# Optimization experiments

Measured on AMD Instinct MI355X. Metric: run time of the kernel, lower is better.

## Reference

```python
import jax, jax.numpy as jnp
import numpy as np

B, N, D, H, DH, DFF = 2, 2048, 1024, 16, 64, 4096
EPS = 1e-5  # F.layer_norm default


def setup_inputs() -> dict:
    key = jax.random.key(0)
    ks = jax.random.split(key, 8)
    w = lambda k, shape: jax.random.normal(k, shape, dtype=jnp.float32) * 0.02
    # standard rotary frequencies over full head dim (rot_dim = DH)
    inv_freq = 1.0 / (10000.0 ** (jnp.arange(0, DH, 2, dtype=jnp.float32) / DH))
    t = jnp.arange(N, dtype=jnp.float32)
    f = t[:, None] * inv_freq[None, :]          # [N, DH/2]
    freqs = jnp.concatenate([f, f], axis=-1)    # [N, DH]
    return {
        "x": jax.random.normal(ks[0], (B, N, D), dtype=jnp.float32),
        "gamma_pre": jnp.ones((D,), jnp.float32),
        "w_qkv": w(ks[1], (3 * D, D)),
        "w_o": w(ks[2], (D, D)),
        "gamma_ff": jnp.ones((D,), jnp.float32),
        "w_up": w(ks[3], (DFF, D)),
        "b_up": jnp.zeros((DFF,), jnp.float32),
        "w_gate": w(ks[4], (DFF, D)),
        "b_gate": jnp.zeros((DFF,), jnp.float32),
        "w_out": w(ks[5], (D, DFF)),
        "b_out": jnp.zeros((D,), jnp.float32),
        "freqs": freqs,
        "mask": jnp.ones((B, N), dtype=bool),
    }


def _layernorm(x, gamma):
    mu = jnp.mean(x, axis=-1, keepdims=True)
    var = jnp.var(x, axis=-1, keepdims=True)
    return (x - mu) * jax.lax.rsqrt(var + EPS) * gamma


def _rotate_half(x):
    x1, x2 = jnp.split(x, 2, axis=-1)
    return jnp.concatenate([-x2, x1], axis=-1)


def _rope(t, freqs):
    # rot_dim == DH so nothing is left unrotated
    return t * jnp.cos(freqs) + _rotate_half(t) * jnp.sin(freqs)


def reference(x, gamma_pre, w_qkv, w_o, gamma_ff, w_up, b_up, w_gate, b_gate,
              w_out, b_out, freqs, mask):
    b, n, d = x.shape
    # ---- self-attention branch (pre-norm) ----
    h = _layernorm(x, gamma_pre)
    qkv = h @ w_qkv.T                                   # [b, n, 3d]
    q, k, v = jnp.split(qkv, 3, axis=-1)
    to_heads = lambda t: t.reshape(b, n, H, DH).transpose(0, 2, 1, 3)  # b h n d
    q, k, v = to_heads(q), to_heads(k), to_heads(v)
    q = _rope(q, freqs)
    k = _rope(k, freqs)
    scale = 1.0 / np.sqrt(DH).astype(np.float32)
    dots = jnp.einsum('bhid,bhjd->bhij', q, k) * scale  # [b, H, n, n]
    neg = -jnp.finfo(dots.dtype).max
    dots = jnp.where(mask[:, None, None, :], dots, neg)        # key padding mask
    causal = jnp.triu(jnp.ones((n, n), dtype=bool), 1)
    dots = jnp.where(causal, neg, dots)
    attn = jax.nn.softmax(dots.astype(jnp.float32), axis=-1).astype(dots.dtype)
    o = jnp.einsum('bhij,bhjd->bhid', attn, v)
    o = o.transpose(0, 2, 1, 3).reshape(b, n, d) @ w_o.T
    o = jnp.where(mask[..., None], o, 0.0)
    x = x + o
    # ---- GLU feed-forward branch (pre-norm) ----
    h2 = _layernorm(x, gamma_ff)
    up = h2 @ w_up.T + b_up
    gate = h2 @ w_gate.T + b_gate
    ff = (up * jax.nn.silu(gate)) @ w_out.T + b_out
    return x + ff
```

## Files before the change

kernel.cpp:

```cpp
#include <hip/hip_runtime.h>
#include <stdint.h>


#define B_ 2
#define N_ 2048
#define D_ 1024
#define H_ 16
#define DFF_ 4096
#define ROWS_ (B_*N_)

typedef unsigned short u16;
typedef short short4_ __attribute__((ext_vector_type(4)));
typedef short short8 __attribute__((ext_vector_type(8)));
typedef float float4_ __attribute__((ext_vector_type(4)));

#define NEGBIG (-1e30f)
#define QSCALE 0.1803368801111204f

__device__ __forceinline__ float b2f(u16 u) {
  union { unsigned u; float f; } c; c.u = ((unsigned)u) << 16; return c.f;
}
__device__ __forceinline__ u16 f2b(float f) {
  union { float f; unsigned u; } c; c.f = f;
  unsigned x = c.u;
// ... 50 lines not shown
  if ((t & 63) == 0) { red[t >> 6] = s; red[4 + (t >> 6)] = ss; }
  __syncthreads();
  s  = red[0] + red[1] + red[2] + red[3];
  ss = red[4] + red[5] + red[6] + red[7];
  float mu  = s * (1.f / D_);
  float var = ss * (1.f / D_) - mu * mu;
  float rs  = rsqrtf(var + 1e-5f);
#pragma unroll
  for (int i = 0; i < 4; i++)
    out[(size_t)row * D_ + t * 4 + i] = f2b((v[i] - mu) * rs * gamma[t * 4 + i]);
}

__global__ __launch_bounds__(256) void combine_ln(const u16* p0,
                                                  const u16* __restrict__ p1,
                                                  const float* __restrict__ resid,
                                                  const float* __restrict__ gamma,
                                                  float* __restrict__ x1,
                                                  u16* h2out) {
  int row = blockIdx.x, t = threadIdx.x;
  size_t base = (size_t)row * D_ + t * 4;
  short4_ a = *(const short4_*)(p0 + base);
  short4_ b = *(const short4_*)(p1 + base);
  float4_ rv = *(const float4_*)(resid + base);
  float4_ v;
  float s = 0.f, ss = 0.f;
#pragma unroll
  for (int i = 0; i < 4; i++) {
    v[i] = b2f((u16)a[i]) + b2f((u16)b[i]) + rv[i];
    s += v[i]; ss += v[i] * v[i];
  }
  *(float4_*)(x1 + base) = v;
#pragma unroll
  for (int off = 1; off < 64; off <<= 1) {
    s  += __shfl_xor(s, off, 64);
    ss += __shfl_xor(ss, off, 64);
  }
  __shared__ float red[8];
  if ((t & 63) == 0) { red[t >> 6] = s; red[4 + (t >> 6)] = ss; }
  __syncthreads();
  s  = red[0] + red[1] + red[2] + red[3];
  ss = red[4] + red[5] + red[6] + red[7];
  float mu  = s * (1.f / D_);
  float var = ss * (1.f / D_) - mu * mu;
  float rs  = rsqrtf(var + 1e-5f);
#pragma unroll
  for (int i = 0; i < 4; i++)
    h2out[base + i] = f2b((v[i] - mu) * rs * gamma[t * 4 + i]);
}

template <int MODE>
__device__ __forceinline__ void gemm_epilogue(float4_ (&acc)[4][4], void* Cout,
                                              const float* bias, const void* extra,
                                              int mbase, int nbase, int N,
                                              int wr, int wc, int quad, int l16) {
#pragma unroll
  for (int i = 0; i < 4; i++) {
#pragma unroll
    for (int r = 0; r < 4; r++) {
      int row = mbase + wr * 64 + i * 16 + quad * 4 + r;
#pragma unroll
      for (int j = 0; j < 4; j++) {
        int col = nbase + wc * 64 + j * 16 + l16;
        size_t idx = (size_t)row * N + col;
        float v = acc[i][j][r];
        if (MODE == 0) {
          ((u16*)Cout)[idx] = f2b(v);
        } else if (MODE == 1) {
          ((u16*)Cout)[idx] = f2b(v + bias[col]);
        } else if (MODE == 2) {
          ((float*)Cout)[idx] = v + ((const float*)extra)[idx];
        } else if (MODE == 3) {
          float gate = v + bias[col];
          float sig = 1.f / (1.f + expf(-gate));
          float upv = b2f(((const u16*)extra)[idx]);
          ((u16*)Cout)[idx] = f2b(upv * gate * sig);
        } else {
          ((float*)Cout)[idx] = v + bias[col] + ((const float*)extra)[idx];
        }
      }
    }
  }
}

__device__ __forceinline__ void gemm_core64(const u16* A, const u16* W,
                                            float4_ (&acc)[4][4], u16* sA, u16* sW,
                                            int mbase, int nbase, int K,
                                            int klo, int khi,
                                            int wave, int lane, int wr, int wc,
                                            int quad, int l16) {
  int colb = ((lane & 3) ^ ((lane >> 3) & 3)) << 3;
  int qs8  = (quad ^ ((l16 >> 1) & 3)) * 8;
  for (int k0 = klo; k0 < khi; k0 += 64) {
    __syncthreads();
#pragma unroll
    for (int hh = 0; hh < 2; hh++) {
      int kh = k0 + hh * 32;
#pragma unroll
      for (int it = 0; it < 2; it++) {
        int c = wave * 128 + it * 64 + lane;
        int row = c >> 2;
        gl_lds16(A + (size_t)(mbase + row) * K + kh + colb,
                 sA + hh * 4096 + (size_t)(wave * 128 + it * 64) * 8);
        gl_lds16(W + (size_t)(nbase + row) * K + kh + colb,
                 sW + hh * 4096 + (size_t)(wave * 128 + it * 64) * 8);
      }
    }
    __syncthreads();
#pragma unroll
    for (int hh = 0; hh < 2; hh++) {
      const u16* sAp = sA + hh * 4096;
      const u16* sWp = sW + hh * 4096;
      short8 af[4], bf[4];
#pragma unroll
      for (int i = 0; i < 4; i++)
        af[i] = *(const short8*)(sAp + (wr * 64 + i * 16 + l16) * 32 + qs8);
#pragma unroll
      for (int j = 0; j < 4; j++)
        bf[j] = *(const short8*)(sWp + (wc * 64 + j * 16 + l16) * 32 + qs8);
#pragma unroll
      for (int i = 0; i < 4; i++)
#pragma unroll
        for (int j = 0; j < 4; j++)
          acc[i][j] = __builtin_amdgcn_mfma_f32_16x16x32_bf16(af[i], bf[j], acc[i][j], 0, 0, 0);
    }
  }
}

__device__ __forceinline__ void glu8_stageA(const u16* A, u16* aslot, int mbase,
                                            int kk, int wave, int lane, int colb) {
  int rw = wave * 16 + (lane >> 2);
#pragma unroll
  for (int it = 0; it < 2; it++) {
    int row = it * 128 + rw;
    gl_lds16(A + (size_t)(mbase + row) * 1024 + kk * 32 + colb,
             aslot + it * 4096 + wave * 512);
  }
}
__device__ __forceinline__ void glu8_stageB(const u16* Wu, const u16* Wg, u16* bslot,
                                            int nbase, int kk, int wave, int lane,
                                            int colb) {
  int rw = wave * 16 + (lane >> 2);
  size_t go = (size_t)(nbase + rw) * 1024 + kk * 32 + colb;
  gl_lds16(Wu + go, bslot + wave * 512);
  gl_lds16(Wg + go, bslot + 4096 + wave * 512);
}

__global__ __launch_bounds__(512) void gemm_glu8(const u16* __restrict__ A,
                                                 const u16* __restrict__ Wu,
                                                 const u16* __restrict__ Wg,
                                                 const float* __restrict__ bu,
                                                 const float* __restrict__ bg,
                                                 u16* __restrict__ G) {
  __shared__ __align__(16) u16 ring[4][16384];
  const int NT = 32;
  int t_ = threadIdx.x, wave = t_ >> 6, lane = t_ & 63;
  int wr = wave >> 2, wc = wave & 3;
  int quad = lane >> 4, l16 = lane & 15;
  int mbase = blockIdx.y * 256, nbase = blockIdx.x * 128;
  int colb = ((lane & 3) ^ ((lane >> 3) & 3)) << 3;
  int qs8  = (quad ^ ((l16 >> 1) & 3)) * 8;

  float4_ z4 = {0.f, 0.f, 0.f, 0.f};
  float4_ acc[8][4];
#pragma unroll
  for (int i = 0; i < 8; i++)
#pragma unroll
    for (int j = 0; j < 4; j++) acc[i][j] = z4;

#pragma unroll
  for (int kk = 0; kk < 3; kk++) {
    glu8_stageA(A, ring[kk], mbase, kk, wave, lane, colb);
    glu8_stageB(Wu, Wg, ring[kk] + 8192, nbase, kk, wave, lane, colb);
  }

  for (int t = 0; t < NT; t++) {
    if (t < NT - 2)       asm volatile("s_waitcnt vmcnt(8)" ::: "memory");
    else if (t == NT - 2) asm volatile("s_waitcnt vmcnt(4)" ::: "memory");
    else                  asm volatile("s_waitcnt vmcnt(0)" ::: "memory");
    __builtin_amdgcn_s_barrier();
    asm volatile("" ::: "memory");

    const u16* as = ring[t & 3];
    const u16* bs = as + 8192;
    bool prefetch = (t + 3 < NT);
    int kk = t + 3;

    if (prefetch) glu8_stageA(A, ring[kk & 3], mbase, kk, wave, lane, colb);
    short8 af[4], bf[4];
#pragma unroll
    for (int i = 0; i < 4; i++)
      af[i] = *(const short8*)(as + (wr * 128 + i * 16 + l16) * 32 + qs8);
#pragma unroll
    for (int j = 0; j < 4; j++)
      bf[j] = *(const short8*)(bs + (wc * 64 + j * 16 + l16) * 32 + qs8);
    __builtin_amdgcn_s_setprio(1);
#pragma unroll
    for (int i = 0; i < 4; i++)
#pragma unroll
      for (int j = 0; j < 4; j++)
        acc[i][j] = __builtin_amdgcn_mfma_f32_16x16x32_bf16(af[i], bf[j], acc[i][j], 0, 0, 0);
    __builtin_amdgcn_s_setprio(0);
    __builtin_amdgcn_s_barrier();
    asm volatile("" ::: "memory");

    if (prefetch) glu8_stageB(Wu, Wg, ring[kk & 3] + 8192, nbase, kk, wave, lane, colb);
    short8 ag[4];
#pragma unroll
    for (int i = 0; i < 4; i++)
      ag[i] = *(const short8*)(as + (wr * 128 + (4 + i) * 16 + l16) * 32 + qs8);
    __builtin_amdgcn_s_setprio(1);
#pragma unroll
    for (int i = 0; i < 4; i++)
#pragma unroll
      for (int j = 0; j < 4; j++)
        acc[4 + i][j] = __builtin_amdgcn_mfma_f32_16x16x32_bf16(ag[i], bf[j], acc[4 + i][j], 0, 0, 0);
    __builtin_amdgcn_s_setprio(0);
  }

  __syncthreads();
  u16* ex = &ring[0][0];
  if (wc >= 2) {
    int cc = (wc - 2) * 64;
#pragma unroll
    for (int i = 0; i < 8; i++)
#pragma unroll
      for (int r = 0; r < 4; r++) {
        int row = wr * 128 + i * 16 + quad * 4 + r;
#pragma unroll
        for (int j = 0; j < 4; j++) {
          int col = cc + j * 16 + l16;
          float gv = acc[i][j][r] + bg[nbase + col];
          float sig = 1.f / (1.f + expf(-gv));
          ex[row * 128 + col] = f2b(gv * sig);
        }
      }
  }
  __syncthreads();
  if (wc < 2) {
    int cc = wc * 64;
#pragma unroll
    for (int i = 0; i < 8; i++)
#pragma unroll
      for (int r = 0; r < 4; r++) {
        int row = wr * 128 + i * 16 + quad * 4 + r;
#pragma unroll
        for (int j = 0; j < 4; j++) {
          int col = cc + j * 16 + l16;
          float uv = acc[i][j][r] + bu[nbase + col];
          G[(size_t)(mbase + row) * DFF_ + nbase + col] =
              f2b(uv * b2f(ex[row * 128 + col]));
        }
      }
  }
}

__global__ __launch_bounds__(256) void gemm_bb_split(const u16* __restrict__ A,
                                                     const u16* __restrict__ W,
                                                     u16* __restrict__ p0,
                                                     u16* __restrict__ p1,
                                                     int M, int N, int K) {
  __shared__ __align__(16) u16 sA[2][128 * 32];
  __shared__ __align__(16) u16 sW[2][128 * 32];
  int t = threadIdx.x;
  int mbase = blockIdx.y * 128, nbase = blockIdx.x * 128;
  int z = blockIdx.z;
  int wave = t >> 6, lane = t & 63;
  int wr = wave >> 1, wc = wave & 1;
  int quad = lane >> 4, l16 = lane & 15;
  int Kh = K >> 1;

  float4_ z4 = {0.f, 0.f, 0.f, 0.f};
  float4_ acc[4][4];
#pragma unroll
  for (int i = 0; i < 4; i++)
#pragma unroll
    for (int j = 0; j < 4; j++) acc[i][j] = z4;

  gemm_core64(A, W, acc, &sA[0][0], &sW[0][0], mbase, nbase, K,
              z * Kh, z * Kh + Kh, wave, lane, wr, wc, quad, l16);

  u16* P = z ? p1 : p0;
#pragma unroll
  for (int i = 0; i < 4; i++)
#pragma unroll
    for (int r = 0; r < 4; r++) {
      int row = mbase + wr * 64 + i * 16 + quad * 4 + r;
#pragma unroll
      for (int j = 0; j < 4; j++) {
        int col = nbase + wc * 64 + j * 16 + l16;
        P[(size_t)row * N + col] = f2b(acc[i][j][r]);
      }
    }
}

__global__ __launch_bounds__(256) void split_combine(const u16* __restrict__ p0,
                                                     const u16* __restrict__ p1,
                                                     const float* __restrict__ bias,
                                                     const float* __restrict__ resid,
                                                     float* __restrict__ out, int N) {
  int idx = (blockIdx.x * 256 + threadIdx.x) * 8;
  int col = idx & (N - 1);
  short8 a = *(const short8*)(p0 + idx);
  short8 b = *(const short8*)(p1 + idx);
  float4_ r0 = *(const float4_*)(resid + idx);
  float4_ r1 = *(const float4_*)(resid + idx + 4);
  float4_ o0, o1;
#pragma unroll
  for (int e = 0; e < 4; e++) {
    float bb0 = bias ? bias[col + e] : 0.f;
    float bb1 = bias ? bias[col + 4 + e] : 0.f;
    o0[e] = b2f((u16)a[e]) + b2f((u16)b[e]) + bb0 + r0[e];
    o1[e] = b2f((u16)a[4 + e]) + b2f((u16)b[4 + e]) + bb1 + r1[e];
  }
  *(float4_*)(out + idx) = o0;
  *(float4_*)(out + idx + 4) = o1;
}

template <int MODE>
__global__ __launch_bounds__(256) void gemm_nt(const u16* __restrict__ A,
                                               const float* __restrict__ W,
                                               void* Cout,
                                               const float* __restrict__ bias,
                                               const void* extra,
                                               int M, int N, int K) {
  __shared__ __align__(16) u16 sA[128 * 32];
  __shared__ __align__(16) u16 sW[128 * 32];
  int t = threadIdx.x;
  int mbase = blockIdx.y * 128, nbase = blockIdx.x * 128;
  int wave = t >> 6, lane = t & 63;
  int wr = wave >> 1, wc = wave & 1;
  int quad = lane >> 4, l16 = lane & 15;

  float4_ z4 = {0.f, 0.f, 0.f, 0.f};
  float4_ acc[4][4];
#pragma unroll
  for (int i = 0; i < 4; i++)
#pragma unroll
    for (int j = 0; j < 4; j++) acc[i][j] = z4;

  for (int k0 = 0; k0 < K; k0 += 32) {
    __syncthreads();
#pragma unroll
    for (int it = 0; it < 2; it++) {
      int c = t + 256 * it;
      int row = c >> 2, col = (c & 3) << 3;
      ((short8*)sA)[c] = *(const short8*)(A + (size_t)(mbase + row) * K + k0 + col);
      const float* wp = W + (size_t)(nbase + row) * K + k0 + col;
      float4_ w0 = *(const float4_*)wp;
      float4_ w1 = *(const float4_*)(wp + 4);
      short8 pk;
#pragma unroll
      for (int e = 0; e < 4; e++) { pk[e] = (short)f2b(w0[e]); pk[4 + e] = (short)f2b(w1[e]); }
      ((short8*)sW)[c] = pk;
    }
    __syncthreads();
    short8 af[4], bf[4];
#pragma unroll
    for (int i = 0; i < 4; i++)
      af[i] = *(const short8*)(sA + (wr * 64 + i * 16 + l16) * 32 + quad * 8);
#pragma unroll
    for (int j = 0; j < 4; j++)
      bf[j] = *(const short8*)(sW + (wc * 64 + j * 16 + l16) * 32 + quad * 8);
#pragma unroll
    for (int i = 0; i < 4; i++)
#pragma unroll
      for (int j = 0; j < 4; j++)
        acc[i][j] = __builtin_amdgcn_mfma_f32_16x16x32_bf16(af[i], bf[j], acc[i][j], 0, 0, 0);
  }
  gemm_epilogue<MODE>(acc, Cout, bias, extra, mbase, nbase, N, wr, wc, quad, l16);
}

template <int SPLIT>
__global__ __launch_bounds__(256) void rope_kernel(const u16* __restrict__ q0,
                                                   const u16* __restrict__ q1,
                                                   const float* __restrict__ freqs,
                                                   u16* __restrict__ qr,
                                                   u16* __restrict__ kr,
                                                   u16* __restrict__ vt) {
  int idx = blockIdx.x * 256 + threadIdx.x;
  int d2 = idx & 31;
  int h  = (idx >> 5) & 15;
  int n  = (idx >> 9) & 2047;
  int b  = idx >> 20;
  float f = freqs[n * 64 + d2];
  float c = cosf(f), s = sinf(f);
  size_t base = (size_t)(b * N_ + n) * 3072;
  int hd = h * 64 + d2;
#define LD(o) (SPLIT ? (b2f(q0[base + (o)]) + b2f(q1[base + (o)])) : b2f(q0[base + (o)]))
  float v_q1 = LD(hd),        v_q2 = LD(hd + 32);
  float v_k1 = LD(1024 + hd), v_k2 = LD(1024 + hd + 32);
  float v_v1 = LD(2048 + hd), v_v2 = LD(2048 + hd + 32);
#undef LD
  size_t ro = ((size_t)(b * H_ + h) * N_ + n) * 64 + d2;
  qr[ro]      = f2b((v_q1 * c - v_q2 * s) * QSCALE);
  qr[ro + 32] = f2b((v_q2 * c + v_q1 * s) * QSCALE);
  kr[ro]      = f2b(v_k1 * c - v_k2 * s);
  kr[ro + 32] = f2b(v_k2 * c + v_k1 * s);
  size_t vo = ((size_t)(b * H_ + h) * 64 + d2) * N_ + n;
  vt[vo]           = f2b(v_v1);
  vt[vo + 32 * N_] = f2b(v_v2);
}

#define LP 72
#define NSPLIT 4
__global__ __launch_bounds__(256) void attn_kernel(const u16* __restrict__ qr,
                                                   const u16* __restrict__ kr,
                                                   const u16* __restrict__ vt,
                                                   u16* __restrict__ opart,
                                                   float* __restrict__ mlp) {
  __shared__ __align__(16) u16 sK[64 * LP];
  __shared__ __align__(16) u16 sV[64 * LP];
  __shared__ __align__(16) u16 sP[4][16 * LP];
  int qp = blockIdx.x, bh = blockIdx.y, sp = blockIdx.z;
  int t = threadIdx.x, wave = t >> 6, lane = t & 63;
  int quad = lane >> 4, l16 = lane & 15;
  const u16* qptr = qr + (size_t)bh * N_ * 64;
  const u16* kp = kr + (size_t)bh * N_ * 64;
  const u16* vp = vt + (size_t)bh * 64 * N_;
  float4_ z4 = {0.f, 0.f, 0.f, 0.f};

  for (int qsel = 0; qsel < 2; qsel++) {
    int qt = qsel ? (N_ / 64 - 1 - qp) : qp;
    int qbase = qt * 64;
    int ntiles = qt + 1;
    int ktlo = (ntiles * sp) / NSPLIT, kthi = (ntiles * (sp + 1)) / NSPLIT;

    short8 aq[2];
    int qrow = qbase + wave * 16 + l16;
#pragma unroll
    for (int kk = 0; kk < 2; kk++)
      aq[kk] = *(const short8*)(qptr + (size_t)qrow * 64 + kk * 32 + quad * 8);

    float4_ o[4] = {z4, z4, z4, z4};
    float m_r[4] = {NEGBIG, NEGBIG, NEGBIG, NEGBIG};
    float l_r[4] = {0.f, 0.f, 0.f, 0.f};

    for (int kt = ktlo; kt < kthi; kt++) {
      __syncthreads();
      {
        const u16* src = kp + (size_t)kt * 64 * 64;
#pragma unroll
        for (int it = 0; it < 2; it++) {
          int c = t + 256 * it;
          int row = c >> 3, seg = c & 7;
          *(short8*)(sK + row * LP + seg * 8) = *(const short8*)(src + c * 8);
          *(short8*)(sV + row * LP + seg * 8) =
              *(const short8*)(vp + (size_t)row * N_ + kt * 64 + seg * 8);
        }
      }
      __syncthreads();

      float4_ sf[4];
#pragma unroll
      for (int j = 0; j < 4; j++) {
        short8 bk0 = *(const short8*)(sK + (j * 16 + l16) * LP + quad * 8);
        short8 bk1 = *(const short8*)(sK + (j * 16 + l16) * LP + 32 + quad * 8);
        float4_ acc = z4;
        acc = __builtin_amdgcn_mfma_f32_16x16x32_bf16(aq[0], bk0, acc, 0, 0, 0);
        acc = __builtin_amdgcn_mfma_f32_16x16x32_bf16(aq[1], bk1, acc, 0, 0, 0);
        sf[j] = acc;
      }
      if (kt == qt) {
#pragma unroll
        for (int j = 0; j < 4; j++)
#pragma unroll
          for (int r = 0; r < 4; r++) {
            int ig = qbase + wave * 16 + quad * 4 + r;
            int jg = kt * 64 + j * 16 + l16;
            if (jg > ig) sf[j][r] = NEGBIG;
          }
      }

#pragma unroll
      for (int r = 0; r < 4; r++) {
        float mt = fmaxf(fmaxf(sf[0][r], sf[1][r]), fmaxf(sf[2][r], sf[3][r]));
#pragma unroll
        for (int off = 1; off < 16; off <<= 1) mt = fmaxf(mt, __shfl_xor(mt, off, 64));
        float mn = fmaxf(m_r[r], mt);
        float alpha = exp2f(m_r[r] - mn);
        float rowsum = 0.f;
#pragma unroll
        for (int j = 0; j < 4; j++) {
          float p = exp2f(sf[j][r] - mn);
          sf[j][r] = p;
          rowsum += p;
        }
#pragma unroll
        for (int off = 1; off < 16; off <<= 1) rowsum += __shfl_xor(rowsum, off, 64);
        l_r[r] = l_r[r] * alpha + rowsum;
        m_r[r] = mn;
#pragma unroll
        for (int jo = 0; jo < 4; jo++) o[jo][r] *= alpha;
      }

      u16* sPw = sP[wave];
#pragma unroll
      for (int j = 0; j < 4; j++)
#pragma unroll
        for (int r = 0; r < 4; r++)
          sPw[(quad * 4 + r) * LP + j * 16 + l16] = f2b(sf[j][r]);
      short8 ap[2];
#pragma unroll
      for (int kk = 0; kk < 2; kk++)
        ap[kk] = *(const short8*)(sPw + l16 * LP + kk * 32 + quad * 8);
#pragma unroll
      for (int jo = 0; jo < 4; jo++)
#pragma unroll
        for (int kk = 0; kk < 2; kk++) {
          short8 bv = *(const short8*)(sV + (jo * 16 + l16) * LP + kk * 32 + quad * 8);
          o[jo] = __builtin_amdgcn_mfma_f32_16x16x32_bf16(ap[kk], bv, o[jo], 0, 0, 0);
        }
    }

#pragma unroll
    for (int r = 0; r < 4; r++) {
      int n = qbase + wave * 16 + quad * 4 + r;
      size_t row = (size_t)bh * N_ + n;
      if (l16 == 0) {
        mlp[2 * (sp * (size_t)65536 + row)]     = m_r[r];
        mlp[2 * (sp * (size_t)65536 + row) + 1] = l_r[r];
      }
#pragma unroll
      for (int jo = 0; jo < 4; jo++)
        opart[sp * (size_t)4194304 + row * 64 + jo * 16 + l16] = f2b(o[jo][r]);
    }
  }
}

__global__ __launch_bounds__(256) void attn_combine(const u16* __restrict__ opart,
                                                    const float* __restrict__ mlp,
                                                    u16* __restrict__ obuf) {
  int idx = blockIdx.x * 256 + threadIdx.x;
  int row = idx >> 3, seg = idx & 7;
  float mm[NSPLIT], ll[NSPLIT];
  float mmax = NEGBIG;
#pragma unroll
  for (int s = 0; s < NSPLIT; s++) {
    mm[s] = mlp[2 * (s * (size_t)65536 + row)];
    ll[s] = mlp[2 * (s * (size_t)65536 + row) + 1];
    mmax = fmaxf(mmax, mm[s]);
  }
  float w[NSPLIT], lsum = 0.f;
#pragma unroll
  for (int s = 0; s < NSPLIT; s++) { w[s] = exp2f(mm[s] - mmax); lsum += ll[s] * w[s]; }
  float inv = 1.f / lsum;
  float acc[8] = {0, 0, 0, 0, 0, 0, 0, 0};
#pragma unroll
  for (int s = 0; s < NSPLIT; s++) {
    short8 a = *(const short8*)(opart + s * (size_t)4194304 + (size_t)row * 64 + seg * 8);
#pragma unroll
    for (int e = 0; e < 8; e++) acc[e] += b2f((u16)a[e]) * w[s];
  }
  short8 r;
#pragma unroll
  for (int e = 0; e < 8; e++) r[e] = (short)f2b(acc[e] * inv);
  int bh = row >> 11, n = row & 2047;
  int bb = bh >> 4, h = bh & 15;
  *(short8*)(obuf + ((size_t)(bb * N_ + n) * D_) + h * 64 + seg * 8) = r;
}

extern "C" void kernel_launch(void* const* d_in, const int* in_sizes, int n_in,
                              void* d_out, int out_size, void* d_ws, size_t ws_size,
                              hipStream_t stream) {
  const float* x         = (const float*)d_in[0];
  const float* gamma_pre = (const float*)d_in[1];
  const float* w_qkv     = (const float*)d_in[2];
  const float* w_o       = (const float*)d_in[3];
  const float* gamma_ff  = (const float*)d_in[4];
  const float* w_up      = (const float*)d_in[5];
  const float* b_up      = (const float*)d_in[6];
  const float* w_gate    = (const float*)d_in[7];
  const float* b_gate    = (const float*)d_in[8];
  const float* w_out     = (const float*)d_in[9];
  const float* b_out     = (const float*)d_in[10];
  const float* freqs     = (const float*)d_in[11];

  char* ws = (char*)d_ws;
  const size_t MB = 1024 * 1024;
  float* out = (float*)d_out;
  bool wide = ws_size >= 96 * MB;

  if (wide) {
    u16*  h     = (u16*)(ws);
    u16*  qp0   = (u16*)(ws + 8 * MB);
    u16*  qp1   = (u16*)(ws + 32 * MB);
    u16*  qr    = (u16*)(ws + 56 * MB);
    u16*  kr    = (u16*)d_out;
    u16*  vtb   = (u16*)d_out + 4194304;
    u16*  opart = (u16*)(ws);
    float* mlb  = (float*)(ws + 32 * MB);
    u16*  ob    = (u16*)(ws + 34 * MB);
    u16*  sp0   = (u16*)(ws);
    u16*  sp1o  = (u16*)(ws + 8 * MB);
    float* x1   = (float*)(ws + 16 * MB);
    u16*  h2    = (u16*)(ws);
    u16*  g     = (u16*)(ws + 32 * MB);
    u16*  sp0f  = (u16*)(ws);
    u16*  sp1f  = (u16*)(ws + 8 * MB);
    u16* wb_qkv  = (u16*)(ws + 64 * MB);
    u16* wb_o    = (u16*)(ws + 70 * MB);
    u16* wb_up   = (u16*)(ws + 72 * MB);
    u16* wb_gate = (u16*)(ws + 80 * MB);
    u16* wb_out  = (u16*)(ws + 88 * MB);

    cvt_all<<<8192, 256, 0, stream>>>(w_qkv, w_o, w_up, w_gate, w_out,
                                      wb_qkv, wb_o, wb_up, wb_gate, wb_out);
    ln_kernel<<<ROWS_, 256, 0, stream>>>(x, gamma_pre, h);
    gemm_bb_split<<<dim3(3072 / 128, ROWS_ / 128, 2), 256, 0, stream>>>(
        h, wb_qkv, qp0, qp1, ROWS_, 3072, 1024);
    rope_kernel<1><<<(B_ * N_ * H_ * 32) / 256, 256, 0, stream>>>(
        qp0, qp1, freqs, qr, kr, vtb);
    attn_kernel<<<dim3(N_ / 128, B_ * H_, NSPLIT), 256, 0, stream>>>(
        qr, kr, vtb, opart, mlb);
    attn_combine<<<(B_ * H_ * N_ * 8) / 256, 256, 0, stream>>>(opart, mlb, ob);
    gemm_bb_split<<<dim3(1024 / 128, ROWS_ / 128, 2), 256, 0, stream>>>(
        ob, wb_o, sp0, sp1o, ROWS_, 1024, 1024);
    combine_ln<<<ROWS_, 256, 0, stream>>>(sp0, sp1o, x, gamma_ff, x1, h2);
    gemm_glu8<<<dim3(DFF_ / 128, ROWS_ / 256), 512, 0, stream>>>(
        h2, wb_up, wb_gate, b_up, b_gate, g);
    gemm_bb_split<<<dim3(1024 / 128, ROWS_ / 128, 2), 256, 0, stream>>>(
        g, wb_out, sp0f, sp1f, ROWS_, 1024, 4096);
    split_combine<<<(ROWS_ * 1024) / 2048, 256, 0, stream>>>(
        sp0f, sp1f, b_out, x1, out, 1024);
  } else {
    u16*  h     = (u16*)(ws);
    u16*  qkv   = (u16*)(ws + 8 * MB);
    u16*  qr    = (u16*)(ws + 32 * MB);
    u16*  kr    = (u16*)(ws + 40 * MB);
    u16*  vtb   = (u16*)(ws + 48 * MB);
    u16*  ob    = (u16*)(ws + 56 * MB);
    float* x1   = (float*)(ws + 8 * MB);
    u16*  h2    = (u16*)(ws + 24 * MB);
    u16*  g     = (u16*)(ws + 32 * MB);

    ln_kernel<<<ROWS_, 256, 0, stream>>>(x, gamma_pre, h);
    gemm_nt<0><<<dim3(3072 / 128, ROWS_ / 128), 256, 0, stream>>>(
        h, w_qkv, qkv, nullptr, nullptr, ROWS_, 3072, 1024);
    rope_kernel<0><<<(B_ * N_ * H_ * 32) / 256, 256, 0, stream>>>(
        qkv, qkv, freqs, qr, kr, vtb);
    attn_kernel<<<dim3(N_ / 128, B_ * H_, NSPLIT), 256, 0, stream>>>(
        qr, kr, vtb, (u16*)(ws), (float*)(ws + 32 * MB));
    attn_combine<<<(B_ * H_ * N_ * 8) / 256, 256, 0, stream>>>(
        (u16*)(ws), (float*)(ws + 32 * MB), ob);
    gemm_nt<2><<<dim3(1024 / 128, ROWS_ / 128), 256, 0, stream>>>(
        ob, w_o, x1, nullptr, x, ROWS_, 1024, 1024);
    ln_kernel<<<ROWS_, 256, 0, stream>>>(x1, gamma_ff, h2);
    gemm_nt<1><<<dim3(4096 / 128, ROWS_ / 128), 256, 0, stream>>>(
        h2, w_up, g, b_up, nullptr, ROWS_, 4096, 1024);
    gemm_nt<3><<<dim3(4096 / 128, ROWS_ / 128), 256, 0, stream>>>(
        h2, w_gate, g, b_gate, g, ROWS_, 4096, 1024);
    gemm_nt<4><<<dim3(1024 / 128, ROWS_ / 128), 256, 0, stream>>>(
        g, w_out, (void*)out, b_out, x1, ROWS_, 1024, 4096);
  }
}
```

Measured before the change: 458.3 us.

## Pipeline split-K GEMM with 4-slot LDS ring and register double-buffered fragments

The split-K GEMM used for the QKV, O and FF-out projections is rebuilt. Instead of a two-barrier load-then-compute loop, it now uses a 4-slot LDS ring with three stages of direct global-to-LDS prefetch and counted vmcnt waits. The GLU GEMM keeps its 4-slot ring, but both kernels now read the next stage's fragments into a second register set while the MFMAs of the current stage run, so LDS reads overlap compute. This costs more registers and LDS, which may lower occupancy.

After: 471.0 us. +2.8%, slower.

```diff
diff --git a/kernel.cpp b/kernel.cpp
--- a/kernel.cpp
+++ b/kernel.cpp
@@ -156,67 +156,97 @@
   }
 }
 
-__device__ __forceinline__ void gemm_core64(const u16* A, const u16* W,
-                                            float4_ (&acc)[4][4], u16* sA, u16* sW,
-                                            int mbase, int nbase, int K,
-                                            int klo, int khi,
-                                            int wave, int lane, int wr, int wc,
-                                            int quad, int l16) {
+__global__ __launch_bounds__(256) void gemm_bb_split(const u16* __restrict__ A,
+                                                     const u16* __restrict__ W,
+                                                     u16* __restrict__ p0,
+                                                     u16* __restrict__ p1,
+                                                     int M, int N, int K) {
+  __shared__ __align__(16) u16 ring[4][8192];
+  int t_ = threadIdx.x, wave = t_ >> 6, lane = t_ & 63;
+  int wr = wave >> 1, wc = wave & 1;
+  int quad = lane >> 4, l16 = lane & 15;
+  int mbase = blockIdx.y * 128, nbase = blockIdx.x * 128;
+  int z = blockIdx.z;
+  int Kh = K >> 1, kbase = z * Kh;
+  const int NT = Kh >> 5;
   int colb = ((lane & 3) ^ ((lane >> 3) & 3)) << 3;
   int qs8  = (quad ^ ((l16 >> 1) & 3)) * 8;
-  for (int k0 = klo; k0 < khi; k0 += 64) {
-    __syncthreads();
-#pragma unroll
-    for (int hh = 0; hh < 2; hh++) {
-      int kh = k0 + hh * 32;
-#pragma unroll
-      for (int it = 0; it < 2; it++) {
-        int c = wave * 128 + it * 64 + lane;
-        int row = c >> 2;
-        gl_lds16(A + (size_t)(mbase + row) * K + kh + colb,
-                 sA + hh * 4096 + (size_t)(wave * 128 + it * 64) * 8);
-        gl_lds16(W + (size_t)(nbase + row) * K + kh + colb,
-                 sW + hh * 4096 + (size_t)(wave * 128 + it * 64) * 8);
-      }
+
+  float4_ z4 = {0.f, 0.f, 0.f, 0.f};
+  float4_ acc[4][4];
+#pragma unroll
+  for (int i = 0; i < 4; i++)
+#pragma unroll
+    for (int j = 0; j < 4; j++) acc[i][j] = z4;
+
+  auto STAGE = [&](int kk) {
+    u16* sl = &ring[kk & 3][0];
+    int kc = kbase + kk * 32 + colb;
+#pragma unroll
+    for (int it = 0; it < 2; it++) {
+      int c = it * 256 + wave * 64 + lane;
+      int row = c >> 2;
+      gl_lds16(A + (size_t)(mbase + row) * K + kc, sl + (it * 256 + wave * 64) * 8);
+      gl_lds16(W + (size_t)(nbase + row) * K + kc, sl + 4096 + (it * 256 + wave * 64) * 8);
     }
-    __syncthreads();
-#pragma unroll
-    for (int hh = 0; hh < 2; hh++) {
-      const u16* sAp = sA + hh * 4096;
-      const u16* sWp = sW + hh * 4096;
-      short8 af[4], bf[4];
-#pragma unroll
-      for (int i = 0; i < 4; i++)
-        af[i] = *(const short8*)(sAp + (wr * 64 + i * 16 + l16) * 32 + qs8);
+  };
+  auto READF = [&](short8 (&fa)[4], short8 (&fb)[4], int kk) {
+    const u16* sl = &ring[kk & 3][0];
+#pragma unroll
+    for (int i = 0; i < 4; i++)
+      fa[i] = *(const short8*)(sl + (wr * 64 + i * 16 + l16) * 32 + qs8);
+#pragma unroll
+    for (int j = 0; j < 4; j++)
+      fb[j] = *(const short8*)(sl + 4096 + (wc * 64 + j * 16 + l16) * 32 + qs8);
+  };
+  auto MM = [&](short8 (&fa)[4], short8 (&fb)[4]) {
+    __builtin_amdgcn_s_setprio(1);
+#pragma unroll
+    for (int i = 0; i < 4; i++)
 #pragma unroll
       for (int j = 0; j < 4; j++)
-        bf[j] = *(const short8*)(sWp + (wc * 64 + j * 16 + l16) * 32 + qs8);
-#pragma unroll
-      for (int i = 0; i < 4; i++)
-#pragma unroll
-        for (int j = 0; j < 4; j++)
-          acc[i][j] = __builtin_amdgcn_mfma_f32_16x16x32_bf16(af[i], bf[j], acc[i][j], 0, 0, 0);
+        acc[i][j] = __builtin_amdgcn_mfma_f32_16x16x32_bf16(fa[i], fb[j], acc[i][j], 0, 0, 0);
+    __builtin_amdgcn_s_setprio(0);
+  };
+
+  STAGE(0); STAGE(1); STAGE(2);
+  asm volatile("s_waitcnt vmcnt(8)" ::: "memory");
+  __builtin_amdgcn_s_barrier();
+  asm volatile("" ::: "memory");
+  short8 aX[4], bX[4], aY[4], bY[4];
+  READF(aX, bX, 0);
+
+  auto ITER = [&](int t, short8 (&ca)[4], short8 (&cb)[4],
+                  short8 (&na)[4], short8 (&nb)[4]) {
+    if (t + 3 < NT) STAGE(t + 3);
+    if (t + 1 < NT) {
+      if (t + 3 < NT)      asm volatile("s_waitcnt vmcnt(8)" ::: "memory");
+      else if (t + 2 < NT) asm volatile("s_waitcnt vmcnt(4)" ::: "memory");
+      else                 asm volatile("s_waitcnt vmcnt(0)" ::: "memory");
+      __builtin_amdgcn_s_barrier();
+      asm volatile("" ::: "memory");
+      READF(na, nb, t + 1);
     }
-  }
-}
-
-__device__ __forceinline__ void glu8_stageA(const u16* A, u16* aslot, int mbase,
-                                            int kk, int wave, int lane, int colb) {
-  int rw = wave * 16 + (lane >> 2);
-#pragma unroll
-  for (int it = 0; it < 2; it++) {
-    int row = it * 128 + rw;
-    gl_lds16(A + (size_t)(mbase + row) * 1024 + kk * 32 + colb,
-             aslot + it * 4096 + wave * 512);
-  }
-}
-__device__ __forceinline__ void glu8_stageB(const u16* Wu, const u16* Wg, u16* bslot,
-                                            int nbase, int kk, int wave, int lane,
-                                            int colb) {
-  int rw = wave * 16 + (lane >> 2);
-  size_t go = (size_t)(nbase + rw) * 1024 + kk * 32 + colb;
-  gl_lds16(Wu + go, bslot + wave * 512);
-  gl_lds16(Wg + go, bslot + 4096 + wave * 512);
+    MM(ca, cb);
+    if (t + 1 < NT) { __builtin_amdgcn_s_barrier(); asm volatile("" ::: "memory"); }
+  };
+  for (int t = 0; t < NT; t += 2) {
+    ITER(t, aX, bX, aY, bY);
+    ITER(t + 1, aY, bY, aX, bX);
+  }
+
+  u16* P = z ? p1 : p0;
+#pragma unroll
+  for (int i = 0; i < 4; i++)
+#pragma unroll
+    for (int r = 0; r < 4; r++) {
+      int row = mbase + wr * 64 + i * 16 + quad * 4 + r;
+#pragma unroll
+      for (int j = 0; j < 4; j++) {
+        int col = nbase + wc * 64 + j * 16 + l16;
+        P[(size_t)row * N + col] = f2b(acc[i][j][r]);
+      }
+    }
 }
 
 __global__ __launch_bounds__(512) void gemm_glu8(const u16* __restrict__ A,
@@ -241,54 +271,62 @@
 #pragma unroll
     for (int j = 0; j < 4; j++) acc[i][j] = z4;
 
-#pragma unroll
-  for (int kk = 0; kk < 3; kk++) {
-    glu8_stageA(A, ring[kk], mbase, kk, wave, lane, colb);
-    glu8_stageB(Wu, Wg, ring[kk] + 8192, nbase, kk, wave, lane, colb);
-  }
-
-  for (int t = 0; t < NT; t++) {
-    if (t < NT - 2)       asm volatile("s_waitcnt vmcnt(8)" ::: "memory");
-    else if (t == NT - 2) asm volatile("s_waitcnt vmcnt(4)" ::: "memory");
-    else                  asm volatile("s_waitcnt vmcnt(0)" ::: "memory");
-    __builtin_amdgcn_s_barrier();
-    asm volatile("" ::: "memory");
-
-    const u16* as = ring[t & 3];
+  auto STAGE = [&](int kk) {
+    u16* sl = &ring[kk & 3][0];
+    int rw = wave * 16 + (lane >> 2);
+    int kc = kk * 32 + colb;
+#pragma unroll
+    for (int it = 0; it < 2; it++)
+      gl_lds16(A + (size_t)(mbase + it * 128 + rw) * 1024 + kc,
+               sl + it * 4096 + wave * 512);
+    size_t go = (size_t)(nbase + rw) * 1024 + kc;
+    gl_lds16(Wu + go, sl + 8192 + wave * 512);
+    gl_lds16(Wg + go, sl + 12288 + wave * 512);
+  };
+  auto READF = [&](short8 (&fa)[8], short8 (&fb)[4], int kk) {
+    const u16* as = &ring[kk & 3][0];
     const u16* bs = as + 8192;
-    bool prefetch = (t + 3 < NT);
-    int kk = t + 3;
-
-    if (prefetch) glu8_stageA(A, ring[kk & 3], mbase, kk, wave, lane, colb);
-    short8 af[4], bf[4];
-#pragma unroll
-    for (int i = 0; i < 4; i++)
-      af[i] = *(const short8*)(as + (wr * 128 + i * 16 + l16) * 32 + qs8);
+#pragma unroll
+    for (int i = 0; i < 8; i++)
+      fa[i] = *(const short8*)(as + (wr * 128 + i * 16 + l16) * 32 + qs8);
 #pragma unroll
     for (int j = 0; j < 4; j++)
-      bf[j] = *(const short8*)(bs + (wc * 64 + j * 16 + l16) * 32 + qs8);
+      fb[j] = *(const short8*)(bs + (wc * 64 + j * 16 + l16) * 32 + qs8);
+  };
+  auto MM = [&](short8 (&fa)[8], short8 (&fb)[4]) {
     __builtin_amdgcn_s_setprio(1);
 #pragma unroll
-    for (int i = 0; i < 4; i++)
+    for (int i = 0; i < 8; i++)
 #pragma unroll
       for (int j = 0; j < 4; j++)
-        acc[i][j] = __builtin_amdgcn_mfma_f32_16x16x32_bf16(af[i], bf[j], acc[i][j], 0, 0, 0);
+        acc[i][j] = __builtin_amdgcn_mfma_f32_16x16x32_bf16(fa[i], fb[j], acc[i][j], 0, 0, 0);
     __builtin_amdgcn_s_setprio(0);
-    __builtin_amdgcn_s_barrier();
-    asm volatile("" ::: "memory");
-
-    if (prefetch) glu8_stageB(Wu, Wg, ring[kk & 3] + 8192, nbase, kk, wave, lane, colb);
-    short8 ag[4];
-#pragma unroll
-    for (int i = 0; i < 4; i++)
-      ag[i] = *(const short8*)(as + (wr * 128 + (4 + i) * 16 + l16) * 32 + qs8);
-    __builtin_amdgcn_s_setprio(1);
-#pragma unroll
-    for (int i = 0; i < 4; i++)
-#pragma unroll
-      for (int j = 0; j < 4; j++)
-        acc[4 + i][j] = __builtin_amdgcn_mfma_f32_16x16x32_bf16(ag[i], bf[j], acc[4 + i][j], 0, 0, 0);
-    __builtin_amdgcn_s_setprio(0);
+  };
+
+  STAGE(0); STAGE(1); STAGE(2);
+  asm volatile("s_waitcnt vmcnt(8)" ::: "memory");
+  __builtin_amdgcn_s_barrier();
+  asm volatile("" ::: "memory");
+  short8 aX[8], bX[4], aY[8], bY[4];
+  READF(aX, bX, 0);
+
+  auto ITER = [&](int t, short8 (&ca)[8], short8 (&cb)[4],
+                  short8 (&na)[8], short8 (&nb)[4]) {
+    if (t + 3 < NT) STAGE(t + 3);
+    if (t + 1 < NT) {
+      if (t + 3 < NT)      asm volatile("s_waitcnt vmcnt(8)" ::: "memory");
+      else if (t + 2 < NT) asm volatile("s_waitcnt vmcnt(4)" ::: "memory");
+      else                 asm volatile("s_waitcnt vmcnt(0)" ::: "memory");
+      __builtin_amdgcn_s_barrier();
+      asm volatile("" ::: "memory");
+      READF(na, nb, t + 1);
+    }
+    MM(ca, cb);
+    if (t + 1 < NT) { __builtin_amdgcn_s_barrier(); asm volatile("" ::: "memory"); }
+  };
+  for (int t = 0; t < NT; t += 2) {
+    ITER(t, aX, bX, aY, bY);
+    ITER(t + 1, aY, bY, aX, bX);
   }
 
   __syncthreads();
@@ -326,45 +364,6 @@
         }
       }
   }
-}
-
-__global__ __launch_bounds__(256) void gemm_bb_split(const u16* __restrict__ A,
-                                                     const u16* __restrict__ W,
-                                                     u16* __restrict__ p0,
-                                                     u16* __restrict__ p1,
-                                                     int M, int N, int K) {
-  __shared__ __align__(16) u16 sA[2][128 * 32];
-  __shared__ __align__(16) u16 sW[2][128 * 32];
-  int t = threadIdx.x;
-  int mbase = blockIdx.y * 128, nbase = blockIdx.x * 128;
-  int z = blockIdx.z;
-  int wave = t >> 6, lane = t & 63;
-  int wr = wave >> 1, wc = wave & 1;
-  int quad = lane >> 4, l16 = lane & 15;
-  int Kh = K >> 1;
-
-  float4_ z4 = {0.f, 0.f, 0.f, 0.f};
-  float4_ acc[4][4];
-#pragma unroll
-  for (int i = 0; i < 4; i++)
-#pragma unroll
-    for (int j = 0; j < 4; j++) acc[i][j] = z4;
-
-  gemm_core64(A, W, acc, &sA[0][0], &sW[0][0], mbase, nbase, K,
-              z * Kh, z * Kh + Kh, wave, lane, wr, wc, quad, l16);
-
-  u16* P = z ? p1 : p0;
-#pragma unroll
-  for (int i = 0; i < 4; i++)
-#pragma unroll
-    for (int r = 0; r < 4; r++) {
-      int row = mbase + wr * 64 + i * 16 + quad * 4 + r;
-#pragma unroll
-      for (int j = 0; j < 4; j++) {
-        int col = nbase + wc * 64 + j * 16 + l16;
-        P[(size_t)row * N + col] = f2b(acc[i][j][r]);
-      }
-    }
 }
 
 __global__ __launch_bounds__(256) void split_combine(const u16* __restrict__ p0,
```

## Double-buffer K/V tiles in attention and remap GEMM block order

Applied to the files above, without the earlier changes.

The attention kernel now prefetches the next K/V tile into registers while computing on the current one, using two LDS buffers, so global load latency overlaps with MFMA work. The number of block barriers per tile stays about the same. The split GEMM and GLU GEMM kernels remap linear block IDs so that groups of 8 consecutive blocks land on different N-columns with the same M-row tiles. This is meant to improve L2 reuse, possibly per-XCD locality. The cost is more register pressure from the prefetched short8 values and extra LDS for the second buffer.

Result: slower. 468.4 us (+2.2%).

```diff
diff --git a/kernel.cpp b/kernel.cpp
--- a/kernel.cpp
+++ b/kernel.cpp
@@ -200,6 +200,50 @@
   }
 }
 
+__global__ __launch_bounds__(256) void gemm_bb_split(const u16* __restrict__ A,
+                                                     const u16* __restrict__ W,
+                                                     u16* __restrict__ p0,
+                                                     u16* __restrict__ p1,
+                                                     int M, int N, int K,
+                                                     int GXC) {
+  __shared__ __align__(16) u16 sA[2][128 * 32];
+  __shared__ __align__(16) u16 sW[2][128 * 32];
+  int t = threadIdx.x;
+  int b = blockIdx.y * (GXC * 8) + blockIdx.x;
+  int grp = b >> 3;
+  int xs = (b & 7) * GXC + (grp >> 5);
+  int ys = grp & 31;
+  int mbase = ys * 128, nbase = xs * 128;
+  int z = blockIdx.z;
+  int wave = t >> 6, lane = t & 63;
+  int wr = wave >> 1, wc = wave & 1;
+  int quad = lane >> 4, l16 = lane & 15;
+  int Kh = K >> 1;
+
+  float4_ z4 = {0.f, 0.f, 0.f, 0.f};
+  float4_ acc[4][4];
+#pragma unroll
+  for (int i = 0; i < 4; i++)
+#pragma unroll
+    for (int j = 0; j < 4; j++) acc[i][j] = z4;
+
+  gemm_core64(A, W, acc, &sA[0][0], &sW[0][0], mbase, nbase, K,
+              z * Kh, z * Kh + Kh, wave, lane, wr, wc, quad, l16);
+
+  u16* P = z ? p1 : p0;
+#pragma unroll
+  for (int i = 0; i < 4; i++)
+#pragma unroll
+    for (int r = 0; r < 4; r++) {
+      int row = mbase + wr * 64 + i * 16 + quad * 4 + r;
+#pragma unroll
+      for (int j = 0; j < 4; j++) {
+        int col = nbase + wc * 64 + j * 16 + l16;
+        P[(size_t)row * N + col] = f2b(acc[i][j][r]);
+      }
+    }
+}
+
 __device__ __forceinline__ void glu8_stageA(const u16* A, u16* aslot, int mbase,
                                             int kk, int wave, int lane, int colb) {
   int rw = wave * 16 + (lane >> 2);
@@ -230,7 +274,11 @@
   int t_ = threadIdx.x, wave = t_ >> 6, lane = t_ & 63;
   int wr = wave >> 2, wc = wave & 3;
   int quad = lane >> 4, l16 = lane & 15;
-  int mbase = blockIdx.y * 256, nbase = blockIdx.x * 128;
+  int b = blockIdx.y * 32 + blockIdx.x;
+  int grp = b >> 3;
+  int xs = (b & 7) * 4 + (grp >> 4);
+  int ys = grp & 15;
+  int mbase = ys * 256, nbase = xs * 128;
   int colb = ((lane & 3) ^ ((lane >> 3) & 3)) << 3;
   int qs8  = (quad ^ ((l16 >> 1) & 3)) * 8;
 
@@ -326,45 +374,6 @@
         }
       }
   }
-}
-
-__global__ __launch_bounds__(256) void gemm_bb_split(const u16* __restrict__ A,
-                                                     const u16* __restrict__ W,
-                                                     u16* __restrict__ p0,
-                                                     u16* __restrict__ p1,
-                                                     int M, int N, int K) {
-  __shared__ __align__(16) u16 sA[2][128 * 32];
-  __shared__ __align__(16) u16 sW[2][128 * 32];
-  int t = threadIdx.x;
-  int mbase = blockIdx.y * 128, nbase = blockIdx.x * 128;
-  int z = blockIdx.z;
-  int wave = t >> 6, lane = t & 63;
-  int wr = wave >> 1, wc = wave & 1;
-  int quad = lane >> 4, l16 = lane & 15;
-  int Kh = K >> 1;
-
-  float4_ z4 = {0.f, 0.f, 0.f, 0.f};
-  float4_ acc[4][4];
-#pragma unroll
-  for (int i = 0; i < 4; i++)
-#pragma unroll
-    for (int j = 0; j < 4; j++) acc[i][j] = z4;
-
-  gemm_core64(A, W, acc, &sA[0][0], &sW[0][0], mbase, nbase, K,
-              z * Kh, z * Kh + Kh, wave, lane, wr, wc, quad, l16);
-
-  u16* P = z ? p1 : p0;
-#pragma unroll
-  for (int i = 0; i < 4; i++)
-#pragma unroll
-    for (int r = 0; r < 4; r++) {
-      int row = mbase + wr * 64 + i * 16 + quad * 4 + r;
-#pragma unroll
-      for (int j = 0; j < 4; j++) {
-        int col = nbase + wc * 64 + j * 16 + l16;
-        P[(size_t)row * N + col] = f2b(acc[i][j][r]);
-      }
-    }
 }
 
 __global__ __launch_bounds__(256) void split_combine(const u16* __restrict__ p0,
@@ -482,8 +491,8 @@
                                                    const u16* __restrict__ vt,
                                                    u16* __restrict__ opart,
                                                    float* __restrict__ mlp) {
-  __shared__ __align__(16) u16 sK[64 * LP];
-  __shared__ __align__(16) u16 sV[64 * LP];
+  __shared__ __align__(16) u16 sK[2][64 * LP];
+  __shared__ __align__(16) u16 sV[2][64 * LP];
   __shared__ __align__(16) u16 sP[4][16 * LP];
   int qp = blockIdx.x, bh = blockIdx.y, sp = blockIdx.z;
   int t = threadIdx.x, wave = t >> 6, lane = t & 63;
@@ -492,6 +501,9 @@
   const u16* kp = kr + (size_t)bh * N_ * 64;
   const u16* vp = vt + (size_t)bh * 64 * N_;
   float4_ z4 = {0.f, 0.f, 0.f, 0.f};
+  int c0 = t, c1 = t + 256;
+  int r0 = c0 >> 3, s0 = (c0 & 7) * 8;
+  int r1 = c1 >> 3, s1 = (c1 & 7) * 8;
 
   for (int qsel = 0; qsel < 2; qsel++) {
     int qt = qsel ? (N_ / 64 - 1 - qp) : qp;
@@ -509,26 +521,27 @@
     float m_r[4] = {NEGBIG, NEGBIG, NEGBIG, NEGBIG};
     float l_r[4] = {0.f, 0.f, 0.f, 0.f};
 
-    for (int kt = ktlo; kt < kthi; kt++) {
-      __syncthreads();
-      {
-        const u16* src = kp + (size_t)kt * 64 * 64;
-#pragma unroll
-        for (int it = 0; it < 2; it++) {
-          int c = t + 256 * it;
-          int row = c >> 3, seg = c & 7;
-          *(short8*)(sK + row * LP + seg * 8) = *(const short8*)(src + c * 8);
-          *(short8*)(sV + row * LP + seg * 8) =
-              *(const short8*)(vp + (size_t)row * N_ + kt * 64 + seg * 8);
-        }
-      }
-      __syncthreads();
-
+    auto LOADR = [&](short8& ka, short8& kb, short8& va, short8& vb, int kt) {
+      const u16* src = kp + (size_t)kt * 4096;
+      ka = *(const short8*)(src + c0 * 8);
+      kb = *(const short8*)(src + c1 * 8);
+      va = *(const short8*)(vp + (size_t)r0 * N_ + kt * 64 + s0);
+      vb = *(const short8*)(vp + (size_t)r1 * N_ + kt * 64 + s1);
+    };
+    auto WRITE = [&](short8& ka, short8& kb, short8& va, short8& vb, int buf) {
+      *(short8*)(sK[buf] + r0 * LP + s0) = ka;
+      *(short8*)(sK[buf] + r1 * LP + s1) = kb;
+      *(short8*)(sV[buf] + r0 * LP + s0) = va;
+      *(short8*)(sV[buf] + r1 * LP + s1) = vb;
+    };
+    auto COMPUTE = [&](int kt, int buf) {
+      const u16* sKb = sK[buf];
+      const u16* sVb = sV[buf];
       float4_ sf[4];
 #pragma unroll
       for (int j = 0; j < 4; j++) {
-        short8 bk0 = *(const short8*)(sK + (j * 16 + l16) * LP + quad * 8);
-        short8 bk1 = *(const short8*)(sK + (j * 16 + l16) * LP + 32 + quad * 8);
+        short8 bk0 = *(const short8*)(sKb + (j * 16 + l16) * LP + quad * 8);
+        short8 bk1 = *(const short8*)(sKb + (j * 16 + l16) * LP + 32 + quad * 8);
         float4_ acc = z4;
         acc = __builtin_amdgcn_mfma_f32_16x16x32_bf16(aq[0], bk0, acc, 0, 0, 0);
         acc = __builtin_amdgcn_mfma_f32_16x16x32_bf16(aq[1], bk1, acc, 0, 0, 0);
@@ -544,7 +557,6 @@
             if (jg > ig) sf[j][r] = NEGBIG;
           }
       }
-
 #pragma unroll
       for (int r = 0; r < 4; r++) {
         float mt = fmaxf(fmaxf(sf[0][r], sf[1][r]), fmaxf(sf[2][r], sf[3][r]));
@@ -566,7 +578,6 @@
 #pragma unroll
         for (int jo = 0; jo < 4; jo++) o[jo][r] *= alpha;
       }
-
       u16* sPw = sP[wave];
 #pragma unroll
       for (int j = 0; j < 4; j++)
@@ -581,9 +592,27 @@
       for (int jo = 0; jo < 4; jo++)
 #pragma unroll
         for (int kk = 0; kk < 2; kk++) {
-          short8 bv = *(const short8*)(sV + (jo * 16 + l16) * LP + kk * 32 + quad * 8);
+          short8 bv = *(const short8*)(sVb + (jo * 16 + l16) * LP + kk * 32 + quad * 8);
           o[jo] = __builtin_amdgcn_mfma_f32_16x16x32_bf16(ap[kk], bv, o[jo], 0, 0, 0);
         }
+    };
+
+    if (ktlo < kthi) {
+      short8 kA0, kA1, vA0, vA1, kB0, kB1, vB0, vB1;
+      LOADR(kA0, kA1, vA0, vA1, ktlo);
+      __syncthreads();
+      for (int kt = ktlo; kt < kthi; kt += 2) {
+        WRITE(kA0, kA1, vA0, vA1, 0);
+        if (kt + 1 < kthi) LOADR(kB0, kB1, vB0, vB1, kt + 1);
+        __syncthreads();
+        COMPUTE(kt, 0);
+        if (kt + 1 < kthi) {
+          WRITE(kB0, kB1, vB0, vB1, 1);
+          if (kt + 2 < kthi) LOADR(kA0, kA1, vA0, vA1, kt + 2);
+          __syncthreads();
+          COMPUTE(kt + 1, 1);
+        }
+      }
     }
 
 #pragma unroll
@@ -681,19 +710,19 @@
                                       wb_qkv, wb_o, wb_up, wb_gate, wb_out);
     ln_kernel<<<ROWS_, 256, 0, stream>>>(x, gamma_pre, h);
     gemm_bb_split<<<dim3(3072 / 128, ROWS_ / 128, 2), 256, 0, stream>>>(
-        h, wb_qkv, qp0, qp1, ROWS_, 3072, 1024);
+        h, wb_qkv, qp0, qp1, ROWS_, 3072, 1024, 3);
     rope_kernel<1><<<(B_ * N_ * H_ * 32) / 256, 256, 0, stream>>>(
         qp0, qp1, freqs, qr, kr, vtb);
     attn_kernel<<<dim3(N_ / 128, B_ * H_, NSPLIT), 256, 0, stream>>>(
         qr, kr, vtb, opart, mlb);
     attn_combine<<<(B_ * H_ * N_ * 8) / 256, 256, 0, stream>>>(opart, mlb, ob);
     gemm_bb_split<<<dim3(1024 / 128, ROWS_ / 128, 2), 256, 0, stream>>>(
-        ob, wb_o, sp0, sp1o, ROWS_, 1024, 1024);
+        ob, wb_o, sp0, sp1o, ROWS_, 1024, 1024, 1);
     combine_ln<<<ROWS_, 256, 0, stream>>>(sp0, sp1o, x, gamma_ff, x1, h2);
     gemm_glu8<<<dim3(DFF_ / 128, ROWS_ / 256), 512, 0, stream>>>(
         h2, wb_up, wb_gate, b_up, b_gate, g);
     gemm_bb_split<<<dim3(1024 / 128, ROWS_ / 128, 2), 256, 0, stream>>>(
-        g, wb_out, sp0f, sp1f, ROWS_, 1024, 4096);
+        g, wb_out, sp0f, sp1f, ROWS_, 1024, 4096, 1);
     split_combine<<<(ROWS_ * 1024) / 2048, 256, 0, stream>>>(
         sp0f, sp1f, b_out, x1, out, 1024);
   } else {
```

## Fuse RoPE and Q/K/V head layout into QKV GEMM epilogue, drop split-K

Applied to the files above, without the earlier changes.

Replaces the split-K QKV GEMM plus the separate rope kernel with a single GEMM that runs the full K=1024 reduction. Its epilogue applies the rotary embedding, the Q scale and the per-head layout, writing V transposed directly. This removes two bf16 partial buffers and one kernel launch. In exchange the grid has half as many blocks, the epilogue computes sin/cos per element, and the transposed V stores are strided.

Measured after the change: 623.8 us. 1.36x slower.

```diff
diff --git a/kernel.cpp b/kernel.cpp
--- a/kernel.cpp
+++ b/kernel.cpp
@@ -200,6 +200,109 @@
   }
 }
 
+__global__ __launch_bounds__(256) void gemm_qkv_rope(const u16* __restrict__ A,
+                                                     const u16* __restrict__ W,
+                                                     const float* __restrict__ freqs,
+                                                     u16* __restrict__ qr,
+                                                     u16* __restrict__ kr,
+                                                     u16* __restrict__ vt) {
+  __shared__ __align__(16) u16 sA[2][128 * 32];
+  __shared__ __align__(16) u16 sW[2][128 * 32];
+  int t = threadIdx.x;
+  int mbase = blockIdx.y * 128, nbase = blockIdx.x * 128;
+  int wave = t >> 6, lane = t & 63;
+  int wr = wave >> 1, wc = wave & 1;
+  int quad = lane >> 4, l16 = lane & 15;
+
+  float4_ z4 = {0.f, 0.f, 0.f, 0.f};
+  float4_ acc[4][4];
+#pragma unroll
+  for (int i = 0; i < 4; i++)
+#pragma unroll
+    for (int j = 0; j < 4; j++) acc[i][j] = z4;
+
+  gemm_core64(A, W, acc, &sA[0][0], &sW[0][0], mbase, nbase, 1024,
+              0, 1024, wave, lane, wr, wc, quad, l16);
+
+  int sec = nbase >> 10;
+  int hbase = ((nbase & 1023) >> 6) + wc;
+  if (sec < 2) {
+    float qs = sec == 0 ? QSCALE : 1.0f;
+    u16* dst = sec == 0 ? qr : kr;
+#pragma unroll
+    for (int i = 0; i < 4; i++) {
+#pragma unroll
+      for (int r = 0; r < 4; r++) {
+        int row = mbase + wr * 64 + i * 16 + quad * 4 + r;
+        int n = row & 2047, bsel = row >> 11;
+        float f0 = freqs[n * 64 + l16];
+        float f1 = freqs[n * 64 + 16 + l16];
+        float c0 = cosf(f0), s0 = sinf(f0);
+        float c1 = cosf(f1), s1 = sinf(f1);
+        size_t base = ((size_t)(bsel * 16 + hbase) * 2048 + n) * 64;
+        float v1a = acc[i][0][r], v2a = acc[i][2][r];
+        float v1b = acc[i][1][r], v2b = acc[i][3][r];
+        dst[base + l16]      = f2b((v1a * c0 - v2a * s0) * qs);
+        dst[base + 16 + l16] = f2b((v1b * c1 - v2b * s1) * qs);
+        dst[base + 32 + l16] = f2b((v2a * c0 + v1a * s0) * qs);
+        dst[base + 48 + l16] = f2b((v2b * c1 + v1b * s1) * qs);
+      }
+    }
+  } else {
+#pragma unroll
+    for (int i = 0; i < 4; i++) {
+#pragma unroll
+      for (int r = 0; r < 4; r++) {
+        int row = mbase + wr * 64 + i * 16 + quad * 4 + r;
+        int n = row & 2047, bsel = row >> 11;
+        size_t vbase = (size_t)(bsel * 16 + hbase) * 64 * 2048;
+#pragma unroll
+        for (int j = 0; j < 4; j++)
+          vt[vbase + (size_t)(j * 16 + l16) * 2048 + n] = f2b(acc[i][j][r]);
+      }
+    }
+  }
+}
+
+__global__ __launch_bounds__(256) void gemm_bb_split(const u16* __restrict__ A,
+                                                     const u16* __restrict__ W,
+                                                     u16* __restrict__ p0,
+                                                     u16* __restrict__ p1,
+                                                     int M, int N, int K) {
+  __shared__ __align__(16) u16 sA[2][128 * 32];
+  __shared__ __align__(16) u16 sW[2][128 * 32];
+  int t = threadIdx.x;
+  int mbase = blockIdx.y * 128, nbase = blockIdx.x * 128;
+  int z = blockIdx.z;
+  int wave = t >> 6, lane = t & 63;
+  int wr = wave >> 1, wc = wave & 1;
+  int quad = lane >> 4, l16 = lane & 15;
+  int Kh = K >> 1;
+
+  float4_ z4 = {0.f, 0.f, 0.f, 0.f};
+  float4_ acc[4][4];
+#pragma unroll
+  for (int i = 0; i < 4; i++)
+#pragma unroll
+    for (int j = 0; j < 4; j++) acc[i][j] = z4;
+
+  gemm_core64(A, W, acc, &sA[0][0], &sW[0][0], mbase, nbase, K,
+              z * Kh, z * Kh + Kh, wave, lane, wr, wc, quad, l16);
+
+  u16* P = z ? p1 : p0;
+#pragma unroll
+  for (int i = 0; i < 4; i++)
+#pragma unroll
+    for (int r = 0; r < 4; r++) {
+      int row = mbase + wr * 64 + i * 16 + quad * 4 + r;
+#pragma unroll
+      for (int j = 0; j < 4; j++) {
+        int col = nbase + wc * 64 + j * 16 + l16;
+        P[(size_t)row * N + col] = f2b(acc[i][j][r]);
+      }
+    }
+}
+
 __device__ __forceinline__ void glu8_stageA(const u16* A, u16* aslot, int mbase,
                                             int kk, int wave, int lane, int colb) {
   int rw = wave * 16 + (lane >> 2);
@@ -326,45 +429,6 @@
         }
       }
   }
-}
-
-__global__ __launch_bounds__(256) void gemm_bb_split(const u16* __restrict__ A,
-                                                     const u16* __restrict__ W,
-                                                     u16* __restrict__ p0,
-                                                     u16* __restrict__ p1,
-                                                     int M, int N, int K) {
-  __shared__ __align__(16) u16 sA[2][128 * 32];
-  __shared__ __align__(16) u16 sW[2][128 * 32];
-  int t = threadIdx.x;
-  int mbase = blockIdx.y * 128, nbase = blockIdx.x * 128;
-  int z = blockIdx.z;
-  int wave = t >> 6, lane = t & 63;
-  int wr = wave >> 1, wc = wave & 1;
-  int quad = lane >> 4, l16 = lane & 15;
-  int Kh = K >> 1;
-
-  float4_ z4 = {0.f, 0.f, 0.f, 0.f};
-  float4_ acc[4][4];
-#pragma unroll
-  for (int i = 0; i < 4; i++)
-#pragma unroll
-    for (int j = 0; j < 4; j++) acc[i][j] = z4;
-
-  gemm_core64(A, W, acc, &sA[0][0], &sW[0][0], mbase, nbase, K,
-              z * Kh, z * Kh + Kh, wave, lane, wr, wc, quad, l16);
-
-  u16* P = z ? p1 : p0;
-#pragma unroll
-  for (int i = 0; i < 4; i++)
-#pragma unroll
-    for (int r = 0; r < 4; r++) {
-      int row = mbase + wr * 64 + i * 16 + quad * 4 + r;
-#pragma unroll
-      for (int j = 0; j < 4; j++) {
-        int col = nbase + wc * 64 + j * 16 + l16;
-        P[(size_t)row * N + col] = f2b(acc[i][j][r]);
-      }
-    }
 }
 
 __global__ __launch_bounds__(256) void split_combine(const u16* __restrict__ p0,
@@ -656,8 +720,6 @@
 
   if (wide) {
     u16*  h     = (u16*)(ws);
-    u16*  qp0   = (u16*)(ws + 8 * MB);
-    u16*  qp1   = (u16*)(ws + 32 * MB);
     u16*  qr    = (u16*)(ws + 56 * MB);
     u16*  kr    = (u16*)d_out;
     u16*  vtb   = (u16*)d_out + 4194304;
@@ -680,10 +742,8 @@
     cvt_all<<<8192, 256, 0, stream>>>(w_qkv, w_o, w_up, w_gate, w_out,
                                       wb_qkv, wb_o, wb_up, wb_gate, wb_out);
     ln_kernel<<<ROWS_, 256, 0, stream>>>(x, gamma_pre, h);
-    gemm_bb_split<<<dim3(3072 / 128, ROWS_ / 128, 2), 256, 0, stream>>>(
-        h, wb_qkv, qp0, qp1, ROWS_, 3072, 1024);
-    rope_kernel<1><<<(B_ * N_ * H_ * 32) / 256, 256, 0, stream>>>(
-        qp0, qp1, freqs, qr, kr, vtb);
+    gemm_qkv_rope<<<dim3(3072 / 128, ROWS_ / 128), 256, 0, stream>>>(
+        h, wb_qkv, freqs, qr, kr, vtb);
     attn_kernel<<<dim3(N_ / 128, B_ * H_, NSPLIT), 256, 0, stream>>>(
         qr, kr, vtb, opart, mlb);
     attn_combine<<<(B_ * H_ * N_ * 8) / 256, 256, 0, stream>>>(opart, mlb, ob);
```
